# Optimization experiments

Hardware: AMD Instinct MI355X
Metric: run time of the kernel (lower is better)

Reference implementation:

```python
import jax, jax.numpy as jnp
import numpy as np

B, L, H, E = 4, 2048, 8, 64
WINDOW = 8
DILATION = 1


def setup_inputs() -> dict:
    key = jax.random.key(0)
    kq, kk, kv, ka = jax.random.split(key, 4)
    queries = jax.random.normal(kq, (B, L, H, E), dtype=jnp.float32)
    keys = jax.random.normal(kk, (B, L, H, E), dtype=jnp.float32)
    values = jax.random.normal(kv, (B, L, H, E), dtype=jnp.float32)
    alpha = jax.random.uniform(ka, (1,), dtype=jnp.float32)
    return {"queries": queries, "keys": keys, "values": values, "alpha": alpha}


def _full_attention(q, k, v, scale):
    # q,k,v: [B, L, H, E]
    scores = jnp.einsum('blhe,bshe->bhls', q, k) * scale  # [B,H,L,L]
    A = jax.nn.softmax(scores, axis=-1)
    return jnp.einsum('bhls,bshd->blhd', A, v)


def _local_attention(q, k, v, scale):
    # efficient gather-based local window attention, non-causal
    Lk = k.shape[1]
    offsets = jnp.arange(-WINDOW, WINDOW + 1) * DILATION
    idx = jnp.clip(jnp.arange(Lk)[:, None] + offsets[None, :], 0, Lk - 1)
    K_win = k[:, idx]
    V_win = v[:, idx]
    scores = jnp.einsum('blhe,blwhe->blhw', q, K_win) * scale
    A = jax.nn.softmax(scores, axis=-1)
    return jnp.einsum('blhw,blwhe->blhe', A, V_win)


def reference(queries, keys, values, alpha):
    scale = 1.0 / np.sqrt(queries.shape[-1]).astype(np.float32)
    out_full = _full_attention(queries, keys, values, scale)
    out_local = _local_attention(queries, keys, values, scale)
    w = jax.nn.sigmoid(alpha[0])
    # only_target_first=True: positions 1..L-1 take out_full, position 0 is gated
    out = out_full.at[:, 0].set(w * out_full[:, 0] + (1.0 - w) * out_local[:, 0])
    return out
```

## Files before the change

### kernel.cpp

```cpp
#include <hip/hip_runtime.h>

typedef unsigned short u16;
typedef unsigned int   u32;
typedef __attribute__((ext_vector_type(8))) short short8;
typedef __attribute__((ext_vector_type(16))) float f32x16;

#define MFMA32(a, b, c) __builtin_amdgcn_mfma_f32_32x32x16_bf16(a, b, c, 0, 0, 0)

constexpr int Lv = 2048, Hv = 8, Ev = 64, HE = Hv * Ev;
constexpr float QSCALE = 0.18033688011112042f;

__device__ __forceinline__ float bf2f(u16 u) {
    u32 x = ((u32)u) << 16;
    return __builtin_bit_cast(float, x);
}
__device__ __forceinline__ u16 f2bf(float f) {
    u32 x = __builtin_bit_cast(u32, f);
    u32 r = ((x >> 16) & 1u) + 0x7fffu;
    return (u16)((x + r) >> 16);
}
__device__ __forceinline__ u32 pkbf(float a, float b) {
#if __has_builtin(__builtin_amdgcn_cvt_pk_bf16_f32)
    typedef __attribute__((ext_vector_type(2))) __bf16 bf16x2;
    bf16x2 v = __builtin_amdgcn_cvt_pk_bf16_f32(a, b);
    return __builtin_bit_cast(u32, v);
#else
    return (u32)f2bf(a) | ((u32)f2bf(b) << 16);
#endif
}
__device__ __forceinline__ float fexp2(float x) {
#if __has_builtin(__builtin_amdgcn_exp2f)
    return __builtin_amdgcn_exp2f(x);
#else
    return exp2f(x);
#endif
}

__device__ __forceinline__ int detect_isbf16(const u32* q32, int lane) {
    u32 w0 = q32[2 * lane];
    u32 w1 = q32[2 * lane + 1];
    u16 uu[4] = { (u16)(w0 & 0xffff), (u16)(w0 >> 16),
                  (u16)(w1 & 0xffff), (u16)(w1 >> 16) };
    int p = 0, z = 0;
#pragma unroll
    for (int j = 0; j < 4; ++j) {
        u16 mgn = (u16)(uu[j] & 0x7fff);
        int ex  = mgn >> 7;
        bool zero = (mgn == 0);
        bool pl   = zero || (ex >= 115 && ex <= 132);
        p += pl ? 1 : 0;
        if ((j & 1) == 0) z += zero ? 1 : 0;
    }
    int acc = p | (z << 16);
#pragma unroll
    for (int o = 1; o < 64; o <<= 1) acc += __shfl_xor(acc, o);
    int ps = acc & 0xffff, zs = acc >> 16;
    if (zs >= 100) return 0;
    return (ps >= 240) ? 1 : 0;
}

__device__ __forceinline__ short8 cvt8s(const float* p, float s) {
    float4 a = *(const float4*)p, b4 = *(const float4*)(p + 4);
    u32 r[4] = { pkbf(a.x * s, a.y * s), pkbf(a.z * s, a.w * s),
                 pkbf(b4.x * s, b4.y * s), pkbf(b4.z * s, b4.w * s) };
    return *(short8*)r;
}

__device__ __forceinline__ f32x16 zv16() {
    f32x16 z;
#pragma unroll
    for (int r = 0; r < 16; ++r) z[r] = 0.f;
    return z;
}

__device__ __forceinline__ void plswap(u32& a, u32& b) {
#if __has_builtin(__builtin_amdgcn_permlane32_swap)
    auto r = __builtin_amdgcn_permlane32_swap(a, b, false, false);
    a = r[0]; b = r[1];
#else
    int lane = (int)(threadIdx.x & 63);
    u32 ax = (u32)__shfl_xor((int)a, 32);
    u32 bx = (u32)__shfl_xor((int)b, 32);
    bool hi = lane >= 32;
    u32 na = hi ? bx : a;
    u32 nb = hi ? b  : ax;
    a = na; b = nb;
#endif
}

template <int ISBF>
__device__ __forceinline__ void attn_impl(
    const void* __restrict__ qv, const void* __restrict__ kv,
    const void* __restrict__ vv, const void* __restrict__ alphav,
    void* __restrict__ outv, u16* Klds, u16* Vt)
{
    const int tid  = threadIdx.x;
    const int w    = tid >> 6;
    const int lane = tid & 63;
    const int l31  = lane & 31;
    const int hi   = lane >> 5;

    const int fid = blockIdx.x;
    const int bh  = (fid & 7) * 4 + ((fid >> 3) & 3);
    const int rb  = fid >> 5;
    const int b   = bh >> 3, h = bh & 7;
    const int row0 = rb * 128;

    const size_t bhoff = (size_t)b * Lv * HE + h * Ev;
    const u16*   q16 = (const u16*)qv + bhoff;
    const u16*   k16 = (const u16*)kv + bhoff;
    const u16*   v16 = (const u16*)vv + bhoff;
    const float* q32 = (const float*)qv + bhoff;
    const float* k32 = (const float*)kv + bhoff;
    const float* v32 = (const float*)vv + bhoff;

    short8 qf[4];
    {
        size_t ro = (size_t)(row0 + w * 32 + l31) * HE + hi * 8;
        if (ISBF) {
#pragma unroll
            for (int c = 0; c < 4; ++c) {
                short8 t = *(const short8*)(q16 + ro + 16 * c);
#pragma unroll
                for (int j = 0; j < 8; ++j)
                    qf[c][j] = (short)f2bf(bf2f((u16)t[j]) * QSCALE);
            }
        } else {
#pragma unroll
            for (int c = 0; c < 4; ++c) qf[c] = cvt8s(q32 + ro + 16 * c, QSCALE);
        }
    }

    f32x16 O[2];
    O[0] = zv16(); O[1] = zv16();
    float psum = 0.f;

    const int kkey = tid >> 3, ksl = tid & 7;
    const int koff = kkey * HE + (ksl ^ (kkey & 7)) * 8;
    const int eq = tid & 15, pp0 = tid >> 4;
    const int kcv0 = pp0 >> 2, pq = pp0 & 3;

    float4 kfa[2], kfb[2], vfa[2], vfb[2];
    uint4  kru[2]; uint2 vru0[2], vru1[2];

#define LOAD_TILE(KT)                                                           \
    do {                                                                        \
        _Pragma("unroll")                                                       \
        for (int i = 0; i < 2; ++i) {                                           \
            if (ISBF) {                                                         \
                kru[i] = *(const uint4*)(k16 + (size_t)(KT) * 64 * HE + koff + i * 32 * HE); \
                const u16* vp_ = v16 + (size_t)((KT) * 64 + 2 * (pp0 + 16 * i)) * HE + eq * 4; \
                vru0[i] = *(const uint2*)vp_;                                   \
                vru1[i] = *(const uint2*)(vp_ + HE);                            \
            } else {                                                            \
                const float* kp_ = k32 + (size_t)(KT) * 64 * HE + koff + i * 32 * HE; \
                kfa[i] = *(const float4*)kp_;                                   \
                kfb[i] = *(const float4*)(kp_ + 4);                             \
                const float* vp_ = v32 + (size_t)((KT) * 64 + 2 * (pp0 + 16 * i)) * HE + eq * 4; \
                vfa[i] = *(const float4*)vp_;                                   \
                vfb[i] = *(const float4*)(vp_ + HE);                            \
            }                                                                   \
        }                                                                       \
    } while (0)

#define STORE_TILE(KB, VB)                                                      \
    do {                                                                        \
        _Pragma("unroll")                                                       \
        for (int i = 0; i < 2; ++i) {                                           \
            if (ISBF) {                                                         \
                *(uint4*)&(KB)[(tid + 256 * i) * 8] = kru[i];                   \
                const u16* a0_ = (const u16*)&vru0[i];                          \
                const u16* a1_ = (const u16*)&vru1[i];                          \
                _Pragma("unroll")                                               \
                for (int j = 0; j < 4; ++j) {                                   \
                    int e_  = eq * 4 + j;                                       \
                    int sl_ = (kcv0 + 4 * i) ^ ((e_ + (e_ >> 3)) & 7);          \
                    u32 val_ = (u32)a0_[j] | ((u32)a1_[j] << 16);               \
                    *(u32*)&(VB)[e_ * 64 + sl_ * 8 + pq * 2] = val_;            \
                }                                                               \
            } else {                                                            \
                u32 kk_[4] = { pkbf(kfa[i].x, kfa[i].y), pkbf(kfa[i].z, kfa[i].w), \
                               pkbf(kfb[i].x, kfb[i].y), pkbf(kfb[i].z, kfb[i].w) }; \
                *(uint4*)&(KB)[(tid + 256 * i) * 8] = *(uint4*)kk_;             \
                float t0_[4] = {vfa[i].x, vfa[i].y, vfa[i].z, vfa[i].w};        \
                float t1_[4] = {vfb[i].x, vfb[i].y, vfb[i].z, vfb[i].w};        \
                _Pragma("unroll")                                               \
                for (int j = 0; j < 4; ++j) {                                   \
                    int e_  = eq * 4 + j;                                       \
                    int sl_ = (kcv0 + 4 * i) ^ ((e_ + (e_ >> 3)) & 7);          \
                    *(u32*)&(VB)[e_ * 64 + sl_ * 8 + pq * 2] = pkbf(t0_[j], t1_[j]); \
                }                                                               \
            }                                                                   \
        }                                                                       \
    } while (0)

    LOAD_TILE(0);
    STORE_TILE(Klds, Vt);
    __syncthreads();

    for (int kt = 0; kt < 32; ++kt) {
        u16* Kb = Klds + (kt & 1) * 4096;
        u16* Vb = Vt   + (kt & 1) * 4096;
        u16* Kn = Klds + ((kt & 1) ^ 1) * 4096;
        u16* Vn = Vt   + ((kt & 1) ^ 1) * 4096;

        if (kt < 31) LOAD_TILE(kt + 1);

        f32x16 St[2];
        St[0] = zv16(); St[1] = zv16();
#pragma unroll
        for (int c = 0; c < 4; ++c) {
#pragma unroll
            for (int s = 0; s < 2; ++s) {
                int krow = s * 32 + l31;
                int sl   = (2 * c + hi) ^ (krow & 7);
                short8 kf = *(const short8*)&Kb[krow * 64 + sl * 8];
                St[s] = MFMA32(kf, qf[c], St[s]);
            }
        }

#pragma unroll
        for (int s = 0; s < 2; ++s) {
            float pe[16];
#pragma unroll
            for (int r = 0; r < 16; ++r) pe[r] = fexp2(St[s][r]);
#pragma unroll
            for (int r = 0; r < 16; ++r) psum += pe[r];
            u32 c8[8];
#pragma unroll
            for (int q = 0; q < 8; ++q) c8[q] = pkbf(pe[2 * q], pe[2 * q + 1]);
#pragma unroll
            for (int t = 0; t < 2; ++t) {
                u32 a0 = c8[4 * t + 0], a1 = c8[4 * t + 1];
                u32 a2 = c8[4 * t + 2], a3 = c8[4 * t + 3];
                plswap(a0, a2);
                plswap(a1, a3);
                u32 pw_[4] = { a0, a1, a2, a3 };
                short8 pa = *(short8*)pw_;
                int ks = 2 * s + t;
#pragma unroll
                for (int et = 0; et < 2; ++et) {
                    int e  = et * 32 + l31;
                    int sl = (2 * ks + hi) ^ ((e + (e >> 3)) & 7);
                    short8 vf = *(const short8*)&Vb[e * 64 + sl * 8];
                    O[et] = MFMA32(pa, vf, O[et]);
                }
            }
        }

        if (kt < 31) {
            STORE_TILE(Kn, Vn);
            __syncthreads();
        }
    }
#undef LOAD_TILE
#undef STORE_TILE

    float locv[2] = {0.f, 0.f};
    float wgt = 0.f;
    const bool w0blk = (rb == 0) && (w == 0);
    if (w0blk) {
        const int e = lane;
        const size_t base = bhoff + e;
#define LDIN(p, i) (ISBF ? bf2f(((const u16*)(p))[i]) : ((const float*)(p))[i])
        float qe = LDIN(qv, base);
        float s[9];
#pragma unroll
        for (int j = 0; j < 9; ++j) {
            float prod = qe * LDIN(kv, base + (size_t)j * HE);
#pragma unroll
            for (int o = 1; o < 64; o <<= 1) prod += __shfl_xor(prod, o);
            s[j] = prod * 0.125f;
        }
        float mx = s[0];
#pragma unroll
        for (int j = 1; j < 9; ++j) mx = fmaxf(mx, s[j]);
        float we[9];
#pragma unroll
        for (int j = 0; j < 9; ++j) we[j] = expf(s[j] - mx);
        float denom = 9.f * we[0];
        float acc   = 9.f * we[0] * LDIN(vv, base);
#pragma unroll
        for (int j = 1; j < 9; ++j) {
            denom += we[j];
            acc   += we[j] * LDIN(vv, base + (size_t)j * HE);
        }
        float loc = acc / denom;

        float a;
        if (ISBF) {
            a = bf2f(((const u16*)alphav)[0]);
            if (!(a >= 0.0f && a <= 1.0f)) {
                float af = ((const float*)alphav)[0];
                if (af >= 0.0f && af <= 1.0f) a = af;
            }
        } else {
            a = ((const float*)alphav)[0];
            if (!(a >= 0.0f && a <= 1.0f)) {
                float ab = bf2f(((const u16*)alphav)[0]);
                if (ab >= 0.0f && ab <= 1.0f) a = ab;
            }
        }
        wgt = 1.f / (1.f + expf(-a));
#pragma unroll
        for (int et = 0; et < 2; ++et) locv[et] = __shfl(loc, et * 32 + l31);
#undef LDIN
    }

    float pst  = psum + __shfl_xor(psum, 32);
    float invv = 1.0f / pst;

#pragma unroll
    for (int rg = 0; rg < 4; ++rg) {
#pragma unroll
        for (int rr = 0; rr < 4; ++rr) {
            const int reg = rg * 4 + rr;
            const int rl  = rr + 8 * rg + 4 * hi;
            float inv = __shfl(invv, rl);
            int row = row0 + w * 32 + rl;
            size_t oo = (size_t)(b * Lv + row) * HE + h * Ev + l31;
            bool blend = w0blk && (rl == 0);
#pragma unroll
            for (int et = 0; et < 2; ++et) {
                float res = O[et][reg] * inv;
                if (blend) res = wgt * res + (1.f - wgt) * locv[et];
                if (ISBF) ((u16*)outv)[oo + et * 32] = f2bf(res);
                else      ((float*)outv)[oo + et * 32] = res;
            }
        }
    }
}

__global__ __launch_bounds__(256, 2) void attn_kernel(
    const void* __restrict__ qv, const void* __restrict__ kv,
    const void* __restrict__ vv, const void* __restrict__ alphav,
    void* __restrict__ outv)
{
    __shared__ u16 Klds[2 * 64 * 64];
    __shared__ u16 Vt[2 * 64 * 64];

    const int isbf = detect_isbf16((const u32*)qv, threadIdx.x & 63);
    if (isbf) attn_impl<1>(qv, kv, vv, alphav, outv, Klds, Vt);
    else      attn_impl<0>(qv, kv, vv, alphav, outv, Klds, Vt);
}

extern "C" void kernel_launch(void* const* d_in, const int* in_sizes, int n_in,
                              void* d_out, int out_size, void* d_ws, size_t ws_size,
                              hipStream_t stream) {
    hipLaunchKernelGGL(attn_kernel, dim3(512), dim3(256), 0, stream,
                       d_in[0], d_in[1], d_in[2], d_in[3], d_out);
}
```

Before: 153.7 us.

## Split key range across warp groups with LDS reduction, halve query tile

Each block now handles 64 query rows instead of 128. Two warp pairs each process half of the key sequence (1024 keys) using 32-key tiles, and their partial O accumulators and row sums are combined through shared memory at the end. The grid doubles to 1024 blocks and the launch bounds request 4 blocks per CU, aiming for better occupancy and latency hiding. The cost is extra K/V global traffic from the smaller query tile, a final LDS reduction with two barriers, and half the warps sitting idle during the output store.

```diff
diff --git a/kernel.cpp b/kernel.cpp
--- a/kernel.cpp
+++ b/kernel.cpp
@@ -92,19 +92,22 @@
 __device__ __forceinline__ void attn_impl(
     const void* __restrict__ qv, const void* __restrict__ kv,
     const void* __restrict__ vv, const void* __restrict__ alphav,
-    void* __restrict__ outv, u16* Klds, u16* Vt)
+    void* __restrict__ outv, u16* SMEM)
 {
     const int tid  = threadIdx.x;
     const int w    = tid >> 6;
     const int lane = tid & 63;
     const int l31  = lane & 31;
     const int hi   = lane >> 5;
+    const int qg   = w & 1;
+    const int g    = w >> 1;
+    const int t7   = tid & 127;
 
     const int fid = blockIdx.x;
     const int bh  = (fid & 7) * 4 + ((fid >> 3) & 3);
     const int rb  = fid >> 5;
     const int b   = bh >> 3, h = bh & 7;
-    const int row0 = rb * 128;
+    const int row0 = rb * 64;
 
     const size_t bhoff = (size_t)b * Lv * HE + h * Ev;
     const u16*   q16 = (const u16*)qv + bhoff;
@@ -114,9 +117,12 @@
     const float* k32 = (const float*)kv + bhoff;
     const float* v32 = (const float*)vv + bhoff;
 
+    u16* Kg = SMEM + g * 4096;
+    u16* Vg = SMEM + 8192 + g * 4096;
+
     short8 qf[4];
     {
-        size_t ro = (size_t)(row0 + w * 32 + l31) * HE + hi * 8;
+        size_t ro = (size_t)(row0 + qg * 32 + l31) * HE + hi * 8;
         if (ISBF) {
 #pragma unroll
             for (int c = 0; c < 4; ++c) {
@@ -135,116 +141,110 @@
     O[0] = zv16(); O[1] = zv16();
     float psum = 0.f;
 
-    const int kkey = tid >> 3, ksl = tid & 7;
-    const int koff = kkey * HE + (ksl ^ (kkey & 7)) * 8;
-    const int eq = tid & 15, pp0 = tid >> 4;
-    const int kcv0 = pp0 >> 2, pq = pp0 & 3;
-
-    float4 kfa[2], kfb[2], vfa[2], vfb[2];
-    uint4  kru[2]; uint2 vru0[2], vru1[2];
+    const int kk0  = t7 >> 3, ks0 = t7 & 7;
+    const int koff = kk0 * HE + ((ks0 ^ (kk0 & 7)) * 8);
+    const int eq = t7 & 7, kp = t7 >> 3;
+    const int kslot = kp >> 2, kpos = kp & 3;
+
+    const size_t gkey = (size_t)g * 1024;
+
+    float4 kfa, kfb, kfc, kfd, vfa, vfb, vfc, vfd;
+    uint4  kru0, kru1, vru0, vru1;
 
 #define LOAD_TILE(KT)                                                           \
     do {                                                                        \
-        _Pragma("unroll")                                                       \
-        for (int i = 0; i < 2; ++i) {                                           \
-            if (ISBF) {                                                         \
-                kru[i] = *(const uint4*)(k16 + (size_t)(KT) * 64 * HE + koff + i * 32 * HE); \
-                const u16* vp_ = v16 + (size_t)((KT) * 64 + 2 * (pp0 + 16 * i)) * HE + eq * 4; \
-                vru0[i] = *(const uint2*)vp_;                                   \
-                vru1[i] = *(const uint2*)(vp_ + HE);                            \
-            } else {                                                            \
-                const float* kp_ = k32 + (size_t)(KT) * 64 * HE + koff + i * 32 * HE; \
-                kfa[i] = *(const float4*)kp_;                                   \
-                kfb[i] = *(const float4*)(kp_ + 4);                             \
-                const float* vp_ = v32 + (size_t)((KT) * 64 + 2 * (pp0 + 16 * i)) * HE + eq * 4; \
-                vfa[i] = *(const float4*)vp_;                                   \
-                vfb[i] = *(const float4*)(vp_ + HE);                            \
+        size_t kb_ = (gkey + (size_t)(KT) * 32) * HE;                           \
+        if (ISBF) {                                                             \
+            kru0 = *(const uint4*)(k16 + kb_ + koff);                           \
+            kru1 = *(const uint4*)(k16 + kb_ + koff + 16 * HE);                 \
+            const u16* vp_ = v16 + kb_ + (size_t)(2 * kp) * HE + eq * 8;        \
+            vru0 = *(const uint4*)vp_;                                          \
+            vru1 = *(const uint4*)(vp_ + HE);                                   \
+        } else {                                                                \
+            const float* kp_ = k32 + kb_ + koff;                                \
+            kfa = *(const float4*)kp_;          kfb = *(const float4*)(kp_ + 4);\
+            kfc = *(const float4*)(kp_ + 16 * HE);                              \
+            kfd = *(const float4*)(kp_ + 16 * HE + 4);                          \
+            const float* vp_ = v32 + kb_ + (size_t)(2 * kp) * HE + eq * 8;      \
+            vfa = *(const float4*)vp_;          vfb = *(const float4*)(vp_ + 4);\
+            vfc = *(const float4*)(vp_ + HE);   vfd = *(const float4*)(vp_ + HE + 4);\
+        }                                                                       \
+    } while (0)
+
+#define STORE_TILE(KB, VB)                                                      \
+    do {                                                                        \
+        if (ISBF) {                                                             \
+            *(uint4*)&(KB)[t7 * 8]         = kru0;                              \
+            *(uint4*)&(KB)[(t7 + 128) * 8] = kru1;                              \
+            const u16* a0_ = (const u16*)&vru0;                                 \
+            const u16* a1_ = (const u16*)&vru1;                                 \
+            _Pragma("unroll")                                                   \
+            for (int j = 0; j < 8; ++j) {                                       \
+                int e_  = eq * 8 + j;                                           \
+                int sl_ = kslot ^ ((e_ + (e_ >> 3)) & 3);                       \
+                u32 val_ = (u32)a0_[j] | ((u32)a1_[j] << 16);                   \
+                *(u32*)&(VB)[e_ * 32 + sl_ * 8 + kpos * 2] = val_;              \
+            }                                                                   \
+        } else {                                                                \
+            u32 k0_[4] = { pkbf(kfa.x, kfa.y), pkbf(kfa.z, kfa.w),              \
+                           pkbf(kfb.x, kfb.y), pkbf(kfb.z, kfb.w) };            \
+            u32 k1_[4] = { pkbf(kfc.x, kfc.y), pkbf(kfc.z, kfc.w),              \
+                           pkbf(kfd.x, kfd.y), pkbf(kfd.z, kfd.w) };            \
+            *(uint4*)&(KB)[t7 * 8]         = *(uint4*)k0_;                      \
+            *(uint4*)&(KB)[(t7 + 128) * 8] = *(uint4*)k1_;                      \
+            float t0_[8] = {vfa.x, vfa.y, vfa.z, vfa.w, vfb.x, vfb.y, vfb.z, vfb.w};\
+            float t1_[8] = {vfc.x, vfc.y, vfc.z, vfc.w, vfd.x, vfd.y, vfd.z, vfd.w};\
+            _Pragma("unroll")                                                   \
+            for (int j = 0; j < 8; ++j) {                                       \
+                int e_  = eq * 8 + j;                                           \
+                int sl_ = kslot ^ ((e_ + (e_ >> 3)) & 3);                       \
+                *(u32*)&(VB)[e_ * 32 + sl_ * 8 + kpos * 2] = pkbf(t0_[j], t1_[j]);\
             }                                                                   \
         }                                                                       \
     } while (0)
 
-#define STORE_TILE(KB, VB)                                                      \
-    do {                                                                        \
-        _Pragma("unroll")                                                       \
-        for (int i = 0; i < 2; ++i) {                                           \
-            if (ISBF) {                                                         \
-                *(uint4*)&(KB)[(tid + 256 * i) * 8] = kru[i];                   \
-                const u16* a0_ = (const u16*)&vru0[i];                          \
-                const u16* a1_ = (const u16*)&vru1[i];                          \
-                _Pragma("unroll")                                               \
-                for (int j = 0; j < 4; ++j) {                                   \
-                    int e_  = eq * 4 + j;                                       \
-                    int sl_ = (kcv0 + 4 * i) ^ ((e_ + (e_ >> 3)) & 7);          \
-                    u32 val_ = (u32)a0_[j] | ((u32)a1_[j] << 16);               \
-                    *(u32*)&(VB)[e_ * 64 + sl_ * 8 + pq * 2] = val_;            \
-                }                                                               \
-            } else {                                                            \
-                u32 kk_[4] = { pkbf(kfa[i].x, kfa[i].y), pkbf(kfa[i].z, kfa[i].w), \
-                               pkbf(kfb[i].x, kfb[i].y), pkbf(kfb[i].z, kfb[i].w) }; \
-                *(uint4*)&(KB)[(tid + 256 * i) * 8] = *(uint4*)kk_;             \
-                float t0_[4] = {vfa[i].x, vfa[i].y, vfa[i].z, vfa[i].w};        \
-                float t1_[4] = {vfb[i].x, vfb[i].y, vfb[i].z, vfb[i].w};        \
-                _Pragma("unroll")                                               \
-                for (int j = 0; j < 4; ++j) {                                   \
-                    int e_  = eq * 4 + j;                                       \
-                    int sl_ = (kcv0 + 4 * i) ^ ((e_ + (e_ >> 3)) & 7);          \
-                    *(u32*)&(VB)[e_ * 64 + sl_ * 8 + pq * 2] = pkbf(t0_[j], t1_[j]); \
-                }                                                               \
-            }                                                                   \
-        }                                                                       \
-    } while (0)
-
     LOAD_TILE(0);
-    STORE_TILE(Klds, Vt);
+    STORE_TILE(Kg, Vg);
     __syncthreads();
 
     for (int kt = 0; kt < 32; ++kt) {
-        u16* Kb = Klds + (kt & 1) * 4096;
-        u16* Vb = Vt   + (kt & 1) * 4096;
-        u16* Kn = Klds + ((kt & 1) ^ 1) * 4096;
-        u16* Vn = Vt   + ((kt & 1) ^ 1) * 4096;
+        u16* Kb = Kg + (kt & 1) * 2048;
+        u16* Vb = Vg + (kt & 1) * 2048;
+        u16* Kn = Kg + ((kt & 1) ^ 1) * 2048;
+        u16* Vn = Vg + ((kt & 1) ^ 1) * 2048;
 
         if (kt < 31) LOAD_TILE(kt + 1);
 
-        f32x16 St[2];
-        St[0] = zv16(); St[1] = zv16();
+        f32x16 St = zv16();
 #pragma unroll
         for (int c = 0; c < 4; ++c) {
-#pragma unroll
-            for (int s = 0; s < 2; ++s) {
-                int krow = s * 32 + l31;
-                int sl   = (2 * c + hi) ^ (krow & 7);
-                short8 kf = *(const short8*)&Kb[krow * 64 + sl * 8];
-                St[s] = MFMA32(kf, qf[c], St[s]);
-            }
-        }
-
-#pragma unroll
-        for (int s = 0; s < 2; ++s) {
-            float pe[16];
-#pragma unroll
-            for (int r = 0; r < 16; ++r) pe[r] = fexp2(St[s][r]);
-#pragma unroll
-            for (int r = 0; r < 16; ++r) psum += pe[r];
-            u32 c8[8];
-#pragma unroll
-            for (int q = 0; q < 8; ++q) c8[q] = pkbf(pe[2 * q], pe[2 * q + 1]);
-#pragma unroll
-            for (int t = 0; t < 2; ++t) {
-                u32 a0 = c8[4 * t + 0], a1 = c8[4 * t + 1];
-                u32 a2 = c8[4 * t + 2], a3 = c8[4 * t + 3];
-                plswap(a0, a2);
-                plswap(a1, a3);
-                u32 pw_[4] = { a0, a1, a2, a3 };
-                short8 pa = *(short8*)pw_;
-                int ks = 2 * s + t;
-#pragma unroll
-                for (int et = 0; et < 2; ++et) {
-                    int e  = et * 32 + l31;
-                    int sl = (2 * ks + hi) ^ ((e + (e >> 3)) & 7);
-                    short8 vf = *(const short8*)&Vb[e * 64 + sl * 8];
-                    O[et] = MFMA32(pa, vf, O[et]);
-                }
+            int sl = (2 * c + hi) ^ (l31 & 7);
+            short8 kf = *(const short8*)&Kb[l31 * 64 + sl * 8];
+            St = MFMA32(kf, qf[c], St);
+        }
+
+        float pe[16];
+#pragma unroll
+        for (int r = 0; r < 16; ++r) pe[r] = fexp2(St[r]);
+#pragma unroll
+        for (int r = 0; r < 16; ++r) psum += pe[r];
+        u32 c8[8];
+#pragma unroll
+        for (int q = 0; q < 8; ++q) c8[q] = pkbf(pe[2 * q], pe[2 * q + 1]);
+#pragma unroll
+        for (int t = 0; t < 2; ++t) {
+            u32 a0 = c8[4 * t + 0], a1 = c8[4 * t + 1];
+            u32 a2 = c8[4 * t + 2], a3 = c8[4 * t + 3];
+            plswap(a0, a2);
+            plswap(a1, a3);
+            u32 pw_[4] = { a0, a1, a2, a3 };
+            short8 pa = *(short8*)pw_;
+#pragma unroll
+            for (int et = 0; et < 2; ++et) {
+                int e  = et * 32 + l31;
+                int sl = (2 * t + hi) ^ ((e + (e >> 3)) & 3);
+                short8 vf = *(const short8*)&Vb[e * 32 + sl * 8];
+                O[et] = MFMA32(pa, vf, O[et]);
             }
         }
 
@@ -255,6 +255,22 @@
     }
 #undef LOAD_TILE
 #undef STORE_TILE
+
+    __syncthreads();
+    float pst = psum + __shfl_xor(psum, 32);
+    float* cb = (float*)SMEM;
+    const int cbase = qg * 2368 + lane * 36;
+
+    if (g == 1) {
+        union { f32x16 v; float4 q4[4]; } u;
+        u.v = O[0];
+#pragma unroll
+        for (int i = 0; i < 4; ++i) *(float4*)&cb[cbase + 4 * i] = u.q4[i];
+        u.v = O[1];
+#pragma unroll
+        for (int i = 0; i < 4; ++i) *(float4*)&cb[cbase + 16 + 4 * i] = u.q4[i];
+        cb[qg * 2368 + 2304 + lane] = pst;
+    }
 
     float locv[2] = {0.f, 0.f};
     float wgt = 0.f;
@@ -307,8 +323,16 @@
 #undef LDIN
     }
 
-    float pst  = psum + __shfl_xor(psum, 32);
-    float invv = 1.0f / pst;
+    __syncthreads();
+    if (g != 0) return;
+
+    float pstp = cb[qg * 2368 + 2304 + lane];
+#pragma unroll
+    for (int r = 0; r < 16; ++r) {
+        O[0][r] += cb[cbase + r];
+        O[1][r] += cb[cbase + 16 + r];
+    }
+    float invv = 1.0f / (pst + pstp);
 
 #pragma unroll
     for (int rg = 0; rg < 4; ++rg) {
@@ -317,7 +341,7 @@
             const int reg = rg * 4 + rr;
             const int rl  = rr + 8 * rg + 4 * hi;
             float inv = __shfl(invv, rl);
-            int row = row0 + w * 32 + rl;
+            int row = row0 + qg * 32 + rl;
             size_t oo = (size_t)(b * Lv + row) * HE + h * Ev + l31;
             bool blend = w0blk && (rl == 0);
 #pragma unroll
@@ -331,22 +355,21 @@
     }
 }
 
-__global__ __launch_bounds__(256, 2) void attn_kernel(
+__global__ __launch_bounds__(256, 4) void attn_kernel(
     const void* __restrict__ qv, const void* __restrict__ kv,
     const void* __restrict__ vv, const void* __restrict__ alphav,
     void* __restrict__ outv)
 {
-    __shared__ u16 Klds[2 * 64 * 64];
-    __shared__ u16 Vt[2 * 64 * 64];
+    __shared__ u16 SMEM[16384];
 
     const int isbf = detect_isbf16((const u32*)qv, threadIdx.x & 63);
-    if (isbf) attn_impl<1>(qv, kv, vv, alphav, outv, Klds, Vt);
-    else      attn_impl<0>(qv, kv, vv, alphav, outv, Klds, Vt);
+    if (isbf) attn_impl<1>(qv, kv, vv, alphav, outv, SMEM);
+    else      attn_impl<0>(qv, kv, vv, alphav, outv, SMEM);
 }
 
 extern "C" void kernel_launch(void* const* d_in, const int* in_sizes, int n_in,
                               void* d_out, int out_size, void* d_ws, size_t ws_size,
                               hipStream_t stream) {
-    hipLaunchKernelGGL(attn_kernel, dim3(512), dim3(256), 0, stream,
+    hipLaunchKernelGGL(attn_kernel, dim3(1024), dim3(256), 0, stream,
                        d_in[0], d_in[1], d_in[2], d_in[3], d_out);
 }
```

Measured after the change: 162.1 us. 1.05x slower.
